# Kernel optimization log

Hardware: AMD Instinct MI355X
Metric: run time of the kernel (lower is better)

## Reference

```python
import jax, jax.numpy as jnp
import numpy as np

B, H, O, T = 4096, 256, 128, 200

def setup_inputs() -> dict:
    key = jax.random.key(0)
    ks = jax.random.split(key, 8)
    s = 1.0 / np.sqrt(H)
    return {
        "C": jax.random.normal(ks[0], (B, H), dtype=jnp.float32),
        "t": jax.random.randint(ks[1], (B,), 0, T),
        "mask": jnp.ones((B, T), dtype=jnp.float32),
        "W_ih": jax.random.uniform(ks[2], (4 * H, H), jnp.float32, -s, s),
        "W_hh": jax.random.uniform(ks[3], (4 * H, H), jnp.float32, -s, s),
        "b_ih": jax.random.uniform(ks[4], (4 * H,), jnp.float32, -s, s),
        "b_hh": jax.random.uniform(ks[5], (4 * H,), jnp.float32, -s, s),
        "W_lin": jax.random.uniform(ks[6], (O, H), jnp.float32, -s, s),
        "b_lin": jax.random.uniform(ks[7], (O,), jnp.float32, -s, s),
    }

def reference(C, t, mask, W_ih, W_hh, b_ih, b_hh, W_lin, b_lin):
    # Input projection is constant across time (same C fed every step).
    x_proj = C @ W_ih.T + b_ih + b_hh  # [B, 4H]
    h0 = jnp.zeros((C.shape[0], W_hh.shape[1]), dtype=C.dtype)
    c0 = jnp.zeros_like(h0)

    def step(carry, _):
        h, c = carry
        gates = x_proj + h @ W_hh.T          # [B, 4H], torch gate order i,f,g,o
        i, f, g, o = jnp.split(gates, 4, axis=-1)
        i = jax.nn.sigmoid(i)
        f = jax.nn.sigmoid(f)
        g = jnp.tanh(g)
        o = jax.nn.sigmoid(o)
        c = f * c + i * g
        h = o * jnp.tanh(c)
        y = h @ W_lin.T + b_lin              # [B, O]
        return (h, c), y

    _, ys = jax.lax.scan(step, (h0, c0), xs=None, length=T)
    return ys  # [T, B, O]
```

## Files before the change

### kernel.cpp

```cpp
#include <hip/hip_runtime.h>


#define B_SZ 4096
#define H_SZ 256
#define O_SZ 128
#define T_SZ 200
#define SW   2032.0f
#define SG   (1.0f/(127.0f*2032.0f))

typedef __bf16 b16x8 __attribute__((ext_vector_type(8)));
typedef float f32x4 __attribute__((ext_vector_type(4)));
typedef int   i32x4 __attribute__((ext_vector_type(4)));
typedef unsigned short u16x8 __attribute__((ext_vector_type(8)));

typedef __attribute__((address_space(1))) const void gas_void;
typedef __attribute__((address_space(3))) void las_void;

__device__ __forceinline__ unsigned short f2bf(float x){
  unsigned u = __builtin_bit_cast(unsigned, x);
  u += 0x7FFFu + ((u >> 16) & 1u);
  return (unsigned short)(u >> 16);
}
__device__ __forceinline__ float bf2f(unsigned short h){
  unsigned u = ((unsigned)h) << 16;
  return __builtin_bit_cast(float, u);
}
__device__ __forceinline__ float fsig(float x){
  float t = __builtin_amdgcn_exp2f(-1.4426950408889634f * x);
  return __builtin_amdgcn_rcpf(1.0f + t);
}
__device__ __forceinline__ float ftanh(float x){
  x = fminf(fmaxf(x, -15.0f), 15.0f);
  float e = __builtin_amdgcn_exp2f(2.8853900817779268f * x);
  return (e - 1.0f) * __builtin_amdgcn_rcpf(e + 1.0f);
}
__device__ __forceinline__ f32x4 mfma16(b16x8 a, b16x8 b, f32x4 c){
  return __builtin_amdgcn_mfma_f32_16x16x32_bf16(a, b, c, 0, 0, 0);
}
__device__ __forceinline__ i32x4 mfma_i8(i32x4 a, i32x4 b, i32x4 c){
  return __builtin_amdgcn_mfma_i32_16x16x64_i8(a, b, c, 0, 0, 0);
}
__device__ __forceinline__ unsigned pk2(float v0, float v1){
  return (unsigned)f2bf(v0) | ((unsigned)f2bf(v1) << 16);
}

__global__ void lstm_setup(const float* __restrict__ Wih, const float* __restrict__ Whh,
                           const float* __restrict__ Wlin, const float* __restrict__ bih,
                           const float* __restrict__ bhh, const float* __restrict__ C,
                           unsigned short* __restrict__ pWih, signed char* __restrict__ qWhh,
                           signed char* __restrict__ qWlin, float* __restrict__ bias,
                           unsigned short* __restrict__ Chi, unsigned short* __restrict__ Clo)
{
  const int nW  = 262144;
  const int nQ  = 262144;
  const int nL  = 32768;
  const int nB  = 1024;
  const int nC  = 1048576;
  long i = (long)blockIdx.x * blockDim.x + threadIdx.x;
  if (i < nW){
    int d = (int)i;
    int j = d & 7, l = (d >> 3) & 63, nt = (d >> 9) & 63, kk = (d >> 15) & 7;
    int src = (nt * 16 + (l & 15)) * H_SZ + kk * 32 + (l >> 4) * 8 + j;
    pWih[d] = f2bf(Wih[src]);
  } else if (i < nW + nQ){
    int d = (int)(i - nW);
    int j = d & 15, l = (d >> 4) & 63, kk = (d >> 10) & 3, nt = d >> 12;
    int n = nt * 16 + (l & 15), k = kk * 64 + (l >> 4) * 16 + j;
    qWhh[d] = (signed char)(int)rintf(Whh[n * H_SZ + k] * SW);
  } else if (i < nW + nQ + nL){
    int d = (int)(i - nW - nQ);
    int j = d & 15, l = (d >> 4) & 63, kk = (d >> 10) & 3, nt = d >> 12;
    int n = nt * 16 + (l & 15), k = kk * 64 + (l >> 4) * 16 + j;
    qWlin[d] = (signed char)(int)rintf(Wlin[n * H_SZ + k] * SW);
  } else if (i < nW + nQ + nL + nB){
    int d = (int)(i - nW - nQ - nL);
    bias[d] = bih[d] + bhh[d];
  } else if (i < nW + nQ + nL + nB + nC){
    int d = (int)(i - nW - nQ - nL - nB);
    float c = C[d];
    unsigned short hi = f2bf(c);
    Chi[d] = hi;
    Clo[d] = f2bf(c - bf2f(hi));
  }
}

__device__ __forceinline__ b16x8 ldsA(const unsigned short* hb, int row, int kbyte){
  int off = row * 512 + (kbyte ^ ((row & 15) << 4));
  return *(const b16x8*)((const char*)hb + off);
}
__device__ __forceinline__ b16x8 ldB2(const unsigned short* __restrict__ p, int ntile, int kk, int l){
  return *(const b16x8*)(p + (((kk * 64 + ntile) << 6) + l) * 8);
}
__device__ __forceinline__ i32x4 ldh(const char* h8, int row, int kbase){
  int off = row * 256 + (kbase ^ ((row & 15) << 4));
  return *(const i32x4*)(h8 + off);
}

__launch_bounds__(512, 1)
__global__ void lstm_main(const unsigned short* __restrict__ pWih,
                          const signed char* __restrict__ qWhh,
                          const signed char* __restrict__ qWlin,
                          const float* __restrict__ bias,
                          const unsigned short* __restrict__ Chi,
                          const unsigned short* __restrict__ Clo,
                          const float* __restrict__ blin,
                          float* __restrict__ out)
{
  __shared__ char smem[4096 + 131072];
  char* h8 = smem;
  char* wl = smem + 4096;
  unsigned short* ctile = (unsigned short*)(smem + 4096);

  const int tid = threadIdx.x;
  const int w = tid >> 6, l = tid & 63;
  const int lm = l & 15, lg = l >> 4;
  const int B0 = blockIdx.x * 16;

  f32x4 accf[8];
  const f32x4 zf = {0.f,0.f,0.f,0.f};
  #pragma unroll
  for (int fi = 0; fi < 8; fi++) accf[fi] = zf;

  for (int pass = 0; pass < 2; pass++){
    const unsigned short* Csrc = pass ? Clo : Chi;
    __syncthreads();
    {
      int r = tid >> 5, c0 = (tid & 31) * 8;
      u16x8 v = *(const u16x8*)(Csrc + (long)(B0 + r) * H_SZ + c0);
      *(u16x8*)((char*)ctile + r * 512 + ((c0 * 2) ^ (r << 4))) = v;
    }
    __syncthreads();
    #pragma unroll
    for (int kk = 0; kk < 8; kk++){
      b16x8 a0 = ldsA(ctile, lm, kk * 64 + lg * 16);
      #pragma unroll
      for (int fi = 0; fi < 8; fi++){
        const int nt = (fi >> 1) * 16 + w * 2 + (fi & 1);
        b16x8 b = ldB2(pWih, nt, kk, l);
        accf[fi] = mfma16(a0, b, accf[fi]);
      }
    }
  }
  unsigned xpb[16];
  #pragma unroll
  for (int fi = 0; fi < 8; fi++){
    const int nt = (fi >> 1) * 16 + w * 2 + (fi & 1);
    float bv = bias[nt * 16 + lm];
    xpb[fi * 2 + 0] = pk2(accf[fi][0] + bv, accf[fi][1] + bv);
    xpb[fi * 2 + 1] = pk2(accf[fi][2] + bv, accf[fi][3] + bv);
  }
  __syncthreads();

  i32x4 bWr[2][8];
  #pragma unroll
  for (int kk = 0; kk < 2; kk++)
    #pragma unroll
    for (int fi = 0; fi < 8; fi++){
      const int nt = (fi >> 1) * 16 + w * 2 + (fi & 1);
      bWr[kk][fi] = *(const i32x4*)(qWhh + (nt * 4 + kk) * 1024 + l * 16);
    }
  #pragma unroll
  for (int kk = 2; kk < 4; kk++)
    #pragma unroll
    for (int fi = 0; fi < 8; fi++){
      const int nt = (fi >> 1) * 16 + w * 2 + (fi & 1);
      __builtin_amdgcn_global_load_lds(
          (gas_void*)(qWhh + (nt * 4 + kk) * 1024 + l * 16),
          (las_void*)(wl + (((w * 2 + (kk - 2)) * 8 + fi) * 1024)), 16, 0, 0);
    }
  i32x4 bL[4];
  #pragma unroll
  for (int kk = 0; kk < 4; kk++)
    bL[kk] = *(const i32x4*)(qWlin + (w * 4 + kk) * 1024 + l * 16);
  float bl = blin[w * 16 + lm];

  float cst[2][4];
  #pragma unroll
  for (int j = 0; j < 2; j++)
    #pragma unroll
    for (int r = 0; r < 4; r++) cst[j][r] = 0.f;

  *(unsigned long long*)(h8 + tid * 8) = 0ull;
  asm volatile("s_waitcnt vmcnt(0) lgkmcnt(0)" ::: "memory");
  __builtin_amdgcn_s_barrier();

  for (int t = 0; t < T_SZ; t++){
    i32x4 acci[8];
    const i32x4 zi = {0,0,0,0};
    #pragma unroll
    for (int fi = 0; fi < 8; fi++) acci[fi] = zi;

    #pragma unroll
    for (int kk = 0; kk < 4; kk++){
      i32x4 a = ldh(h8, lm, kk * 64 + lg * 16);
      #pragma unroll
      for (int fi = 0; fi < 8; fi++){
        i32x4 b;
        if (kk < 2) b = bWr[kk][fi];
        else        b = *(const i32x4*)(wl + (((w * 2 + (kk - 2)) * 8 + fi) * 1024) + l * 16);
        acci[fi] = mfma_i8(a, b, acci[fi]);
      }
    }
    asm volatile("s_waitcnt lgkmcnt(0)" ::: "memory");
    __builtin_amdgcn_s_barrier();

    #pragma unroll
    for (int j = 0; j < 2; j++)
      #pragma unroll
      for (int r = 0; r < 4; r++){
        unsigned ui = xpb[(0 * 2 + j) * 2 + (r >> 1)];
        unsigned uf = xpb[(1 * 2 + j) * 2 + (r >> 1)];
        unsigned ug = xpb[(2 * 2 + j) * 2 + (r >> 1)];
        unsigned uo = xpb[(3 * 2 + j) * 2 + (r >> 1)];
        float xi = __builtin_bit_cast(float, (r & 1) ? (ui & 0xFFFF0000u) : (ui << 16));
        float xf = __builtin_bit_cast(float, (r & 1) ? (uf & 0xFFFF0000u) : (uf << 16));
        float xg = __builtin_bit_cast(float, (r & 1) ? (ug & 0xFFFF0000u) : (ug << 16));
        float xo = __builtin_bit_cast(float, (r & 1) ? (uo & 0xFFFF0000u) : (uo << 16));
        float iv = fsig (SG * (float)acci[0 + j][r] + xi);
        float fv = fsig (SG * (float)acci[2 + j][r] + xf);
        float gv = ftanh(SG * (float)acci[4 + j][r] + xg);
        float ov = fsig (SG * (float)acci[6 + j][r] + xo);
        float cn = fv * cst[j][r] + iv * gv;
        cst[j][r] = cn;
        float hv = ov * ftanh(cn);
        int row = lg * 4 + r;
        int col = w * 32 + j * 16 + lm;
        h8[row * 256 + (col ^ (row << 4))] = (signed char)(int)rintf(hv * 127.0f);
      }
    asm volatile("s_waitcnt lgkmcnt(0)" ::: "memory");
    __builtin_amdgcn_s_barrier();

    i32x4 ya = zi;
    #pragma unroll
    for (int kk = 0; kk < 4; kk++){
      i32x4 a = ldh(h8, lm, kk * 64 + lg * 16);
      ya = mfma_i8(a, bL[kk], ya);
    }
    float* op = out + (long)t * (B_SZ * O_SZ) + (long)B0 * O_SZ;
    #pragma unroll
    for (int r = 0; r < 4; r++){
      int row = lg * 4 + r;
      __builtin_nontemporal_store(SG * (float)ya[r] + bl, op + row * O_SZ + w * 16 + lm);
    }
  }
}

extern "C" void kernel_launch(void* const* d_in, const int* in_sizes, int n_in,
                              void* d_out, int out_size, void* d_ws, size_t ws_size,
                              hipStream_t stream)
{
  const float* C    = (const float*)d_in[0];
  const float* Wih  = (const float*)d_in[3];
  const float* Whh  = (const float*)d_in[4];
  const float* bih  = (const float*)d_in[5];
  const float* bhh  = (const float*)d_in[6];
  const float* Wlin = (const float*)d_in[7];
  const float* blin = (const float*)d_in[8];
  float* out = (float*)d_out;

  char* ws = (char*)d_ws;
  unsigned short* pWih = (unsigned short*)(ws);
  signed char*    qWhh = (signed char*)(ws + 524288);
  signed char*    qWlin= (signed char*)(ws + 786432);
  float*          bias = (float*)(ws + 819200);
  unsigned short* Chi  = (unsigned short*)(ws + 823296);
  unsigned short* Clo  = (unsigned short*)(ws + 2920448);

  int total = 262144 + 262144 + 32768 + 1024 + 1048576;
  lstm_setup<<<dim3((total + 255) / 256), dim3(256), 0, stream>>>(
      Wih, Whh, Wlin, bih, bhh, C, pWih, qWhh, qWlin, bias, Chi, Clo);
  lstm_main<<<dim3(256), dim3(512), 0, stream>>>(
      pWih, qWhh, qWlin, bias, Chi, Clo, blin, out);
}
```

Baseline: 408.0 us.

## Double LSTM block to 16 waves, keep all recurrent weights in registers

The main kernel now runs 1024 threads per block instead of 512, so each wave owns one 16-column tile per gate instead of two. All of W_hh is held in registers, which removes the per-step LDS reads of half the recurrent weights, and the output-projection weights move into LDS for the first 8 waves. The input projection is kept in fp32 registers instead of packed bf16, which drops the unpack work and is slightly more precise. The cost is a lower per-wave register budget at 1024 threads and idle waves during the output projection.

New measurement: 410.1 us. Within noise of the previous version (+0.5%).

```diff
diff --git a/kernel.cpp b/kernel.cpp
--- a/kernel.cpp
+++ b/kernel.cpp
@@ -39,9 +39,6 @@
 }
 __device__ __forceinline__ i32x4 mfma_i8(i32x4 a, i32x4 b, i32x4 c){
   return __builtin_amdgcn_mfma_i32_16x16x64_i8(a, b, c, 0, 0, 0);
-}
-__device__ __forceinline__ unsigned pk2(float v0, float v1){
-  return (unsigned)f2bf(v0) | ((unsigned)f2bf(v1) << 16);
 }
 
 __global__ void lstm_setup(const float* __restrict__ Wih, const float* __restrict__ Whh,
@@ -96,7 +93,7 @@
   return *(const i32x4*)(h8 + off);
 }
 
-__launch_bounds__(512, 1)
+__launch_bounds__(1024, 1)
 __global__ void lstm_main(const unsigned short* __restrict__ pWih,
                           const signed char* __restrict__ qWhh,
                           const signed char* __restrict__ qWlin,
@@ -106,9 +103,9 @@
                           const float* __restrict__ blin,
                           float* __restrict__ out)
 {
-  __shared__ char smem[4096 + 131072];
+  __shared__ char smem[4096 + 32768];
   char* h8 = smem;
-  char* wl = smem + 4096;
+  char* wlin = smem + 4096;
   unsigned short* ctile = (unsigned short*)(smem + 4096);
 
   const int tid = threadIdx.x;
@@ -116,15 +113,15 @@
   const int lm = l & 15, lg = l >> 4;
   const int B0 = blockIdx.x * 16;
 
-  f32x4 accf[8];
+  f32x4 accf[4];
   const f32x4 zf = {0.f,0.f,0.f,0.f};
   #pragma unroll
-  for (int fi = 0; fi < 8; fi++) accf[fi] = zf;
+  for (int g = 0; g < 4; g++) accf[g] = zf;
 
   for (int pass = 0; pass < 2; pass++){
     const unsigned short* Csrc = pass ? Clo : Chi;
     __syncthreads();
-    {
+    if (tid < 512){
       int r = tid >> 5, c0 = (tid & 31) * 8;
       u16x8 v = *(const u16x8*)(Csrc + (long)(B0 + r) * H_SZ + c0);
       *(u16x8*)((char*)ctile + r * 512 + ((c0 * 2) ^ (r << 4))) = v;
@@ -134,113 +131,88 @@
     for (int kk = 0; kk < 8; kk++){
       b16x8 a0 = ldsA(ctile, lm, kk * 64 + lg * 16);
       #pragma unroll
-      for (int fi = 0; fi < 8; fi++){
-        const int nt = (fi >> 1) * 16 + w * 2 + (fi & 1);
-        b16x8 b = ldB2(pWih, nt, kk, l);
-        accf[fi] = mfma16(a0, b, accf[fi]);
+      for (int g = 0; g < 4; g++){
+        b16x8 b = ldB2(pWih, g * 16 + w, kk, l);
+        accf[g] = mfma16(a0, b, accf[g]);
       }
     }
   }
-  unsigned xpb[16];
-  #pragma unroll
-  for (int fi = 0; fi < 8; fi++){
-    const int nt = (fi >> 1) * 16 + w * 2 + (fi & 1);
-    float bv = bias[nt * 16 + lm];
-    xpb[fi * 2 + 0] = pk2(accf[fi][0] + bv, accf[fi][1] + bv);
-    xpb[fi * 2 + 1] = pk2(accf[fi][2] + bv, accf[fi][3] + bv);
+  f32x4 xpf[4];
+  #pragma unroll
+  for (int g = 0; g < 4; g++){
+    float bv = bias[(g * 16 + w) * 16 + lm];
+    #pragma unroll
+    for (int r = 0; r < 4; r++) xpf[g][r] = accf[g][r] + bv;
   }
   __syncthreads();
 
-  i32x4 bWr[2][8];
-  #pragma unroll
-  for (int kk = 0; kk < 2; kk++)
-    #pragma unroll
-    for (int fi = 0; fi < 8; fi++){
-      const int nt = (fi >> 1) * 16 + w * 2 + (fi & 1);
-      bWr[kk][fi] = *(const i32x4*)(qWhh + (nt * 4 + kk) * 1024 + l * 16);
-    }
-  #pragma unroll
-  for (int kk = 2; kk < 4; kk++)
-    #pragma unroll
-    for (int fi = 0; fi < 8; fi++){
-      const int nt = (fi >> 1) * 16 + w * 2 + (fi & 1);
-      __builtin_amdgcn_global_load_lds(
-          (gas_void*)(qWhh + (nt * 4 + kk) * 1024 + l * 16),
-          (las_void*)(wl + (((w * 2 + (kk - 2)) * 8 + fi) * 1024)), 16, 0, 0);
-    }
-  i32x4 bL[4];
-  #pragma unroll
-  for (int kk = 0; kk < 4; kk++)
-    bL[kk] = *(const i32x4*)(qWlin + (w * 4 + kk) * 1024 + l * 16);
-  float bl = blin[w * 16 + lm];
-
-  float cst[2][4];
-  #pragma unroll
-  for (int j = 0; j < 2; j++)
-    #pragma unroll
-    for (int r = 0; r < 4; r++) cst[j][r] = 0.f;
-
-  *(unsigned long long*)(h8 + tid * 8) = 0ull;
+  i32x4 bW[4][4];
+  #pragma unroll
+  for (int g = 0; g < 4; g++)
+    #pragma unroll
+    for (int kk = 0; kk < 4; kk++)
+      bW[g][kk] = *(const i32x4*)(qWhh + ((g * 16 + w) * 4 + kk) * 1024 + l * 16);
+  #pragma unroll
+  for (int f = 0; f < 2; f++)
+    __builtin_amdgcn_global_load_lds(
+        (gas_void*)(qWlin + (w * 2 + f) * 1024 + l * 16),
+        (las_void*)(wlin + (w * 2 + f) * 1024 + l * 16), 16, 0, 0);
+  float bl = (w < 8) ? blin[w * 16 + lm] : 0.f;
+
+  float cst[4];
+  #pragma unroll
+  for (int r = 0; r < 4; r++) cst[r] = 0.f;
+
+  *(unsigned*)(h8 + tid * 4) = 0u;
   asm volatile("s_waitcnt vmcnt(0) lgkmcnt(0)" ::: "memory");
   __builtin_amdgcn_s_barrier();
 
   for (int t = 0; t < T_SZ; t++){
-    i32x4 acci[8];
+    i32x4 acci[4];
     const i32x4 zi = {0,0,0,0};
     #pragma unroll
-    for (int fi = 0; fi < 8; fi++) acci[fi] = zi;
+    for (int g = 0; g < 4; g++) acci[g] = zi;
 
     #pragma unroll
     for (int kk = 0; kk < 4; kk++){
       i32x4 a = ldh(h8, lm, kk * 64 + lg * 16);
       #pragma unroll
-      for (int fi = 0; fi < 8; fi++){
-        i32x4 b;
-        if (kk < 2) b = bWr[kk][fi];
-        else        b = *(const i32x4*)(wl + (((w * 2 + (kk - 2)) * 8 + fi) * 1024) + l * 16);
-        acci[fi] = mfma_i8(a, b, acci[fi]);
-      }
+      for (int g = 0; g < 4; g++)
+        acci[g] = mfma_i8(a, bW[g][kk], acci[g]);
     }
     asm volatile("s_waitcnt lgkmcnt(0)" ::: "memory");
     __builtin_amdgcn_s_barrier();
 
     #pragma unroll
-    for (int j = 0; j < 2; j++)
-      #pragma unroll
-      for (int r = 0; r < 4; r++){
-        unsigned ui = xpb[(0 * 2 + j) * 2 + (r >> 1)];
-        unsigned uf = xpb[(1 * 2 + j) * 2 + (r >> 1)];
-        unsigned ug = xpb[(2 * 2 + j) * 2 + (r >> 1)];
-        unsigned uo = xpb[(3 * 2 + j) * 2 + (r >> 1)];
-        float xi = __builtin_bit_cast(float, (r & 1) ? (ui & 0xFFFF0000u) : (ui << 16));
-        float xf = __builtin_bit_cast(float, (r & 1) ? (uf & 0xFFFF0000u) : (uf << 16));
-        float xg = __builtin_bit_cast(float, (r & 1) ? (ug & 0xFFFF0000u) : (ug << 16));
-        float xo = __builtin_bit_cast(float, (r & 1) ? (uo & 0xFFFF0000u) : (uo << 16));
-        float iv = fsig (SG * (float)acci[0 + j][r] + xi);
-        float fv = fsig (SG * (float)acci[2 + j][r] + xf);
-        float gv = ftanh(SG * (float)acci[4 + j][r] + xg);
-        float ov = fsig (SG * (float)acci[6 + j][r] + xo);
-        float cn = fv * cst[j][r] + iv * gv;
-        cst[j][r] = cn;
-        float hv = ov * ftanh(cn);
-        int row = lg * 4 + r;
-        int col = w * 32 + j * 16 + lm;
-        h8[row * 256 + (col ^ (row << 4))] = (signed char)(int)rintf(hv * 127.0f);
-      }
+    for (int r = 0; r < 4; r++){
+      float iv = fsig (SG * (float)acci[0][r] + xpf[0][r]);
+      float fv = fsig (SG * (float)acci[1][r] + xpf[1][r]);
+      float gv = ftanh(SG * (float)acci[2][r] + xpf[2][r]);
+      float ov = fsig (SG * (float)acci[3][r] + xpf[3][r]);
+      float cn = fv * cst[r] + iv * gv;
+      cst[r] = cn;
+      float hv = ov * ftanh(cn);
+      int row = lg * 4 + r;
+      int col = w * 16 + lm;
+      h8[row * 256 + (col ^ (row << 4))] = (signed char)(int)rintf(hv * 127.0f);
+    }
     asm volatile("s_waitcnt lgkmcnt(0)" ::: "memory");
     __builtin_amdgcn_s_barrier();
 
-    i32x4 ya = zi;
-    #pragma unroll
-    for (int kk = 0; kk < 4; kk++){
-      i32x4 a = ldh(h8, lm, kk * 64 + lg * 16);
-      ya = mfma_i8(a, bL[kk], ya);
-    }
-    float* op = out + (long)t * (B_SZ * O_SZ) + (long)B0 * O_SZ;
-    #pragma unroll
-    for (int r = 0; r < 4; r++){
-      int row = lg * 4 + r;
-      __builtin_nontemporal_store(SG * (float)ya[r] + bl, op + row * O_SZ + w * 16 + lm);
+    if (w < 8){
+      i32x4 ya = zi;
+      #pragma unroll
+      for (int kk = 0; kk < 4; kk++){
+        i32x4 a  = ldh(h8, lm, kk * 64 + lg * 16);
+        i32x4 bb = *(const i32x4*)(wlin + (w * 4 + kk) * 1024 + l * 16);
+        ya = mfma_i8(a, bb, ya);
+      }
+      float* op = out + (long)t * (B_SZ * O_SZ) + (long)B0 * O_SZ;
+      #pragma unroll
+      for (int r = 0; r < 4; r++){
+        int row = lg * 4 + r;
+        __builtin_nontemporal_store(SG * (float)ya[r] + bl, op + row * O_SZ + w * 16 + lm);
+      }
     }
   }
 }
@@ -269,6 +241,6 @@
   int total = 262144 + 262144 + 32768 + 1024 + 1048576;
   lstm_setup<<<dim3((total + 255) / 256), dim3(256), 0, stream>>>(
       Wih, Whh, Wlin, bih, bhh, C, pWih, qWhh, qWlin, bias, Chi, Clo);
-  lstm_main<<<dim3(256), dim3(512), 0, stream>>>(
+  lstm_main<<<dim3(256), dim3(1024), 0, stream>>>(
       pWih, qWhh, qWlin, bias, Chi, Clo, blin, out);
 }
```
